# Performance work log

Hardware: AMD Instinct MI355X
Metric: run time of the kernel (lower is better)

## Reference

```python
import jax, jax.numpy as jnp
import numpy as np

B, L, D, M = 8, 4096, 512, 64


def setup_inputs() -> dict:
    key = jax.random.key(0)
    k1, k2, k3 = jax.random.split(key, 3)
    scale = 1.0 / (D * D)
    return {
        "q": jax.random.normal(k1, (B, L, D), dtype=jnp.float32),
        "w_real": scale * jax.random.normal(k2, (D, D, M), dtype=jnp.float32),
        "w_imag": scale * jax.random.normal(k3, (D, D, M), dtype=jnp.float32),
    }


def reference(q, w_real, w_imag):
    # q: [B, L, D]; weights: [D, D, modes]
    b, l, d = q.shape
    n_freq = l // 2 + 1
    q_ft = jnp.fft.rfft(q, axis=1)                      # [B, n_freq, D] complex64
    m = min(w_real.shape[-1], n_freq)
    W = w_real[..., :m] + 1j * w_imag[..., :m]          # [D, E, m] complex
    # Batched over modes: replaces the per-mode python loop with one einsum.
    out_m = jnp.einsum('bmd,dem->bme', q_ft[:, :m, :], W)  # [B, m, D]
    out_ft = jnp.zeros((b, n_freq, d), dtype=q_ft.dtype).at[:, :m, :].set(out_m)
    return jnp.fft.irfft(out_ft, n=l, axis=1)           # [B, L, D] float32
```

## Files before the change

kernel.cpp:

```cpp
#include <hip/hip_runtime.h>

#define B_ 8
#define L_ 4096
#define D_ 512
#define M_ 64

typedef __attribute__((ext_vector_type(8))) short bh8;
typedef __attribute__((ext_vector_type(4))) float f4;
typedef __attribute__((ext_vector_type(4))) unsigned u32x4;

__device__ inline unsigned short f2bf(float f) {
  unsigned u = __float_as_uint(f);
  return (unsigned short)((u + 0x7fffu + ((u >> 16) & 1u)) >> 16);
}
__device__ inline unsigned packbf(float lo, float hi) {
  return (unsigned)f2bf(lo) | ((unsigned)f2bf(hi) << 16);
}

__global__ void k_ftab(unsigned short* __restrict__ F) {
  int t = blockIdx.x * 256 + threadIdx.x;
  int r = t >> 12, l = t & 4095;
  int k = r & 63, part = r >> 6;
  int ph = (k * l) & (L_ - 1);
  double ang = 6.283185307179586476925286766559 * (double)ph / (double)L_;
  float v = part ? (float)(-sin(ang)) : (float)(cos(ang));
  F[t] = f2bf(v);
}

__global__ void k_gtab(unsigned short* __restrict__ G) {
  int t = blockIdx.x * 256 + threadIdx.x;
  int l = t >> 7, j = t & 127;
  int k = j & 63, part = j >> 6;
  int ph = (k * l) & (L_ - 1);
  double ang = 6.283185307179586476925286766559 * (double)ph / (double)L_;
  double ck = (k == 0 ? 1.0 : 2.0) / (double)L_;
  float v = part ? (float)(-ck * sin(ang)) : (float)(ck * cos(ang));
  G[t] = f2bf(v);
}

__global__ __launch_bounds__(512, 4) void k_dft_mfma(
    const float* __restrict__ q, const unsigned short* __restrict__ F,
    float* __restrict__ pQ) {
  int tid = threadIdx.x;
  int dt = blockIdx.x, b = blockIdx.y, kc = blockIdx.z;
  int d0 = dt * 64;
  int lbase = kc * 512;

  int w = tid >> 6, lane = tid & 63;
  int mh = w & 3, nc = w >> 2;
  int lr = lane & 15, kg = lane >> 4;

  f4 acc[2][2];
#pragma unroll
  for (int i = 0; i < 2; ++i)
#pragma unroll
    for (int j = 0; j < 2; ++j) { f4 z = {0.f, 0.f, 0.f, 0.f}; acc[i][j] = z; }

  const unsigned short* A0 = F + (size_t)(mh * 32 + lr) * 4096 + lbase + kg * 8;
  const unsigned short* A1 = A0 + (size_t)16 * 4096;
  const float* q0 = q + ((size_t)b * L_ + lbase + kg * 8) * D_ + d0 + nc * 32 + lr;

#pragma unroll 2
  for (int s = 0; s < 16; ++s) {
    const float* qs = q0 + (size_t)s * 32 * D_;
    float v0[8], v1[8];
#pragma unroll
    for (int j = 0; j < 8; ++j) {
      v0[j] = qs[(size_t)j * D_];
      v1[j] = qs[(size_t)j * D_ + 16];
    }
    union { u32x4 u; bh8 h; } bf0, bf1;
    bf0.u.x = packbf(v0[0], v0[1]); bf0.u.y = packbf(v0[2], v0[3]);
    bf0.u.z = packbf(v0[4], v0[5]); bf0.u.w = packbf(v0[6], v0[7]);
    bf1.u.x = packbf(v1[0], v1[1]); bf1.u.y = packbf(v1[2], v1[3]);
    bf1.u.z = packbf(v1[4], v1[5]); bf1.u.w = packbf(v1[6], v1[7]);
    bh8 af0 = *(const bh8*)(A0 + s * 32);
    bh8 af1 = *(const bh8*)(A1 + s * 32);
    acc[0][0] = __builtin_amdgcn_mfma_f32_16x16x32_bf16(af0, bf0.h, acc[0][0], 0, 0, 0);
    acc[0][1] = __builtin_amdgcn_mfma_f32_16x16x32_bf16(af0, bf1.h, acc[0][1], 0, 0, 0);
    acc[1][0] = __builtin_amdgcn_mfma_f32_16x16x32_bf16(af1, bf0.h, acc[1][0], 0, 0, 0);
    acc[1][1] = __builtin_amdgcn_mfma_f32_16x16x32_bf16(af1, bf1.h, acc[1][1], 0, 0, 0);
  }

#pragma unroll
  for (int mi = 0; mi < 2; ++mi) {
    int r = mh * 32 + mi * 16 + kg * 4;
#pragma unroll
    for (int ni = 0; ni < 2; ++ni) {
      int d = d0 + nc * 32 + ni * 16 + lr;
#pragma unroll
      for (int j = 0; j < 4; ++j)
        pQ[(((size_t)kc * 128 + (r + j)) * 8 + b) * 512 + d] = acc[mi][ni][j];
    }
  }
}

__global__ __launch_bounds__(256) void k_red2(const float* __restrict__ pQ,
                                              unsigned* __restrict__ Qbf) {
  int g = blockIdx.x * 256 + threadIdx.x;
  int dq = g & 127;
  int b = (g >> 7) & 7;
  int k = g >> 10;
  f4 sr = {0.f, 0.f, 0.f, 0.f}, si = {0.f, 0.f, 0.f, 0.f};
#pragma unroll
  for (int kc = 0; kc < 8; ++kc) {
    size_t base = (((size_t)kc * 128 + k) * 8 + b) * 512 + dq * 4;
    sr += *(const f4*)(pQ + base);
    si += *(const f4*)(pQ + base + (size_t)64 * 8 * 512);
  }
  u32x4 o;
  o.x = packbf(sr[0], si[0]); o.y = packbf(sr[1], si[1]);
  o.z = packbf(sr[2], si[2]); o.w = packbf(sr[3], si[3]);
  *(u32x4*)(Qbf + ((size_t)k * 8 + b) * 512 + dq * 4) = o;
}

__global__ __launch_bounds__(256, 5) void k_mix_mfma(
    const float* __restrict__ wr_, const float* __restrict__ wi_,
    const unsigned* __restrict__ Qbf, float* __restrict__ pOut) {
  __shared__ unsigned Wt[4096];

  int tid = threadIdx.x;
  int et = blockIdx.x, dc = blockIdx.y, kq = blockIdx.z;
  int e0 = et * 16, D0 = dc * 32, k0 = kq * 16;
  int w = tid >> 6, lane = tid & 63;
  int er = lane & 15, kg = lane >> 4;
  int part = er >> 3, b = er & 7;

  int se = tid & 15;
  int sk4 = (tid >> 4) & 3;
  int sdg = tid >> 6;

  f4 acc[4];
#pragma unroll
  for (int t = 0; t < 4; ++t) { f4 z = {0.f, 0.f, 0.f, 0.f}; acc[t] = z; }

#pragma unroll 1
  for (int r = 0; r < 2; ++r) {
    if (r) __syncthreads();
#pragma unroll
    for (int i = 0; i < 4; ++i) {
      int dl = sdg * 4 + i;
      size_t dd = (size_t)(D0 + r * 16 + dl);
      size_t gb = (dd * 512 + e0 + se) * 64 + k0 + sk4 * 4;
      float4 vr = *(const float4*)(wr_ + gb);
      float4 vi = *(const float4*)(wi_ + gb);
      int dp = dl ^ (sk4 << 2);
      unsigned* o = &Wt[(sk4 * 4) * 256 + se * 16 + dp];
      o[0]   = packbf(vr.x, vi.x);
      o[256] = packbf(vr.y, vi.y);
      o[512] = packbf(vr.z, vi.z);
      o[768] = packbf(vr.w, vi.w);
    }
    __syncthreads();
#pragma unroll
    for (int t = 0; t < 4; ++t) {
      int kl = w * 4 + t;
      int sw = (kl >> 2) << 2;
      union { u32x4 u; bh8 h; } av, bv;
      av.u = *(const u32x4*)&Wt[kl * 256 + er * 16 + ((kg * 4) ^ sw)];
      u32x4 qv = *(const u32x4*)(Qbf +
          ((size_t)(k0 + kl) * 8 + b) * 512 + D0 + r * 16 + kg * 4);
      if (part == 0) {
        bv.u.x = qv.x ^ 0x80000000u; bv.u.y = qv.y ^ 0x80000000u;
        bv.u.z = qv.z ^ 0x80000000u; bv.u.w = qv.w ^ 0x80000000u;
      } else {
        bv.u.x = (qv.x >> 16) | (qv.x << 16); bv.u.y = (qv.y >> 16) | (qv.y << 16);
        bv.u.z = (qv.z >> 16) | (qv.z << 16); bv.u.w = (qv.w >> 16) | (qv.w << 16);
      }
      acc[t] = __builtin_amdgcn_mfma_f32_16x16x32_bf16(av.h, bv.h, acc[t], 0, 0, 0);
    }
  }

#pragma unroll
  for (int t = 0; t < 4; ++t) {
    int kglob = k0 + w * 4 + t;
    size_t off = (size_t)dc * 524288 +
                 (((size_t)kglob * 2 + part) * 8 + b) * 512 + e0 + kg * 4;
    *(f4*)(pOut + off) = acc[t];
  }
}

__global__ __launch_bounds__(256) void k_psum2(const float* __restrict__ pOut,
                                               unsigned* __restrict__ Pw) {
  __shared__ float sP[128 * 33];
  int tid = threadIdx.x;
  int e0 = blockIdx.x * 32, b = blockIdx.y;
  {
    int e = tid & 31, kg4 = tid >> 5;
#pragma unroll
    for (int ii = 0; ii < 16; ++ii) {
      int col = kg4 * 16 + ii;
      int rkp = ((col & 63) << 1) | (col >> 6);
      float s = 0.f;
#pragma unroll
      for (int c = 0; c < 16; ++c)
        s += pOut[(size_t)c * 524288 + (size_t)rkp * 4096 + b * 512 + e0 + e];
      sP[col * 33 + e] = s;
    }
  }
  __syncthreads();
  {
    int e = tid >> 3, c = tid & 7;
    size_t wbase = (((size_t)b * 512 + e0 + e) * 128 + c * 16) >> 1;
#pragma unroll
    for (int ii = 0; ii < 8; ++ii) {
      int col = c * 16 + ii * 2;
      Pw[wbase + ii] = packbf(sP[col * 33 + e], sP[(col + 1) * 33 + e]);
    }
  }
}

#define LST 72
__global__ __launch_bounds__(256, 2) void k_inv_mfma(
    const short* __restrict__ G, const short* __restrict__ P,
    float* __restrict__ y) {
  __shared__ short lds[2 * 128 * LST];
  short* As = lds;
  short* Bs = lds + 128 * LST;

  int tid = threadIdx.x;
  int lt = blockIdx.x, et = blockIdx.y, b = blockIdx.z;
  int l0 = lt * 128, e0 = et * 128;

  int wv = tid >> 6, lane = tid & 63;
  int wrow = wv >> 1, wcol = wv & 1;
  int lr = lane & 15, kg = lane >> 4;

  const short* Gb = G + (size_t)l0 * 128;
  const short* Pb = P + (size_t)b * D_ * 128 + (size_t)e0 * 128;

  f4 acc[4][4];
#pragma unroll
  for (int mi = 0; mi < 4; ++mi)
#pragma unroll
    for (int ni = 0; ni < 4; ++ni) {
      f4 z = {0.f, 0.f, 0.f, 0.f};
      acc[mi][ni] = z;
    }

#pragma unroll
  for (int kh = 0; kh < 2; ++kh) {
    if (kh) __syncthreads();
#pragma unroll
    for (int i = 0; i < 4; ++i) {
      int idx = i * 256 + tid;
      int row = idx >> 3, c = idx & 7;
      *(uint4*)(As + row * LST + c * 8) =
          *(const uint4*)(Gb + (size_t)row * 128 + kh * 64 + c * 8);
      *(uint4*)(Bs + row * LST + c * 8) =
          *(const uint4*)(Pb + (size_t)row * 128 + kh * 64 + c * 8);
    }
    __syncthreads();

#pragma unroll
    for (int ks = 0; ks < 2; ++ks) {
      bh8 a[4], bf[4];
#pragma unroll
      for (int i = 0; i < 4; ++i) {
        a[i]  = *(const bh8*)(As + (wrow * 64 + i * 16 + lr) * LST + ks * 32 + kg * 8);
        bf[i] = *(const bh8*)(Bs + (wcol * 64 + i * 16 + lr) * LST + ks * 32 + kg * 8);
      }
#pragma unroll
      for (int mi = 0; mi < 4; ++mi)
#pragma unroll
        for (int ni = 0; ni < 4; ++ni)
          acc[mi][ni] = __builtin_amdgcn_mfma_f32_16x16x32_bf16(
              a[mi], bf[ni], acc[mi][ni], 0, 0, 0);
    }
  }

#pragma unroll
  for (int mi = 0; mi < 4; ++mi) {
    int lg = l0 + wrow * 64 + mi * 16 + kg * 4;
#pragma unroll
    for (int ni = 0; ni < 4; ++ni) {
      int e = e0 + wcol * 64 + ni * 16 + lr;
#pragma unroll
      for (int j = 0; j < 4; ++j)
        y[((size_t)b * L_ + (lg + j)) * D_ + e] = acc[mi][ni][j];
    }
  }
}

extern "C" void kernel_launch(void* const* d_in, const int* in_sizes, int n_in,
                              void* d_out, int out_size, void* d_ws, size_t ws_size,
                              hipStream_t stream) {
  const float* q  = (const float*)d_in[0];
  const float* wr = (const float*)d_in[1];
  const float* wi = (const float*)d_in[2];
  float* out = (float*)d_out;
  char* ws = (char*)d_ws;

  unsigned short* Fbf = (unsigned short*)ws;
  unsigned short* Gbf = (unsigned short*)(ws + (1u << 20));
  unsigned* Qbf       = (unsigned*)(ws + (2u << 20));
  unsigned* Pw        = (unsigned*)(ws + (3u << 20));

  float* pQ   = out;
  float* pOut = out;

  hipLaunchKernelGGL(k_ftab, dim3((128 * L_) / 256), dim3(256), 0, stream, Fbf);
  hipLaunchKernelGGL(k_gtab, dim3((L_ * 128) / 256), dim3(256), 0, stream, Gbf);
  hipLaunchKernelGGL(k_dft_mfma, dim3(8, 8, 8), dim3(512), 0, stream,
                     q, Fbf, pQ);
  hipLaunchKernelGGL(k_red2, dim3(65536 / 256), dim3(256), 0, stream, pQ, Qbf);
  hipLaunchKernelGGL(k_mix_mfma, dim3(32, 16, 4), dim3(256), 0, stream,
                     wr, wi, Qbf, pOut);
  hipLaunchKernelGGL(k_psum2, dim3(16, 8), dim3(256), 0, stream, pOut, Pw);
  hipLaunchKernelGGL(k_inv_mfma, dim3(L_ / 128, D_ / 128, B_), dim3(256), 0,
                     stream, (const short*)Gbf, (const short*)Pw, out);
}
```

Before: 113.7 us.

## Give each wave a private LDS weight tile in the mode-mixing kernel

Restructures the mode-mixing MFMA kernel so that each wave stages its own 16-mode by 16-channel weight slab into a private LDS buffer. Cross-wave __syncthreads is replaced by a waitcnt-based fence. Each wave now accumulates 16 MFMA tiles instead of 4, and the grid shrinks from 2048 to 512 blocks. The goal is to remove block-wide barriers and raise the number of global weight loads in flight per thread. In exchange it uses four times the LDS and more accumulator registers, which lowers occupancy, and it keeps 16 partial-sum slices over D.

```diff
diff --git a/kernel.cpp b/kernel.cpp
--- a/kernel.cpp
+++ b/kernel.cpp
@@ -114,52 +114,70 @@
   *(u32x4*)(Qbf + ((size_t)k * 8 + b) * 512 + dq * 4) = o;
 }
 
-__global__ __launch_bounds__(256, 5) void k_mix_mfma(
+__global__ __launch_bounds__(256, 2) void k_mix_mfma(
     const float* __restrict__ wr_, const float* __restrict__ wi_,
     const unsigned* __restrict__ Qbf, float* __restrict__ pOut) {
-  __shared__ unsigned Wt[4096];
+  __shared__ unsigned Wlds[4 * 4096];
 
   int tid = threadIdx.x;
-  int et = blockIdx.x, dc = blockIdx.y, kq = blockIdx.z;
-  int e0 = et * 16, D0 = dc * 32, k0 = kq * 16;
+  int et = blockIdx.x, dc = blockIdx.y, kh = blockIdx.z;
+  int e0 = et * 16;
   int w = tid >> 6, lane = tid & 63;
   int er = lane & 15, kg = lane >> 4;
   int part = er >> 3, b = er & 7;
-
-  int se = tid & 15;
-  int sk4 = (tid >> 4) & 3;
-  int sdg = tid >> 6;
-
-  f4 acc[4];
-#pragma unroll
-  for (int t = 0; t < 4; ++t) { f4 z = {0.f, 0.f, 0.f, 0.f}; acc[t] = z; }
+  int dh = w & 1;
+  int ksl = kh * 32 + (w >> 1) * 16;
+  unsigned* wbuf = Wlds + w * 4096;
+
+  int dL = lane >> 4;
+  int eL = (lane >> 2) & 3;
+  int kq = lane & 3;
+
+  f4 acc[16];
+#pragma unroll
+  for (int t = 0; t < 16; ++t) { f4 z = {0.f, 0.f, 0.f, 0.f}; acc[t] = z; }
+
+  const unsigned* qbase = Qbf + ((size_t)ksl * 8 + b) * 512 + kg * 4;
+
+#define DSFENCE() do {                                        \
+    asm volatile("s_waitcnt lgkmcnt(0)" ::: "memory");        \
+    __builtin_amdgcn_sched_barrier(0);                        \
+  } while (0)
 
 #pragma unroll 1
   for (int r = 0; r < 2; ++r) {
-    if (r) __syncthreads();
-#pragma unroll
-    for (int i = 0; i < 4; ++i) {
-      int dl = sdg * 4 + i;
-      size_t dd = (size_t)(D0 + r * 16 + dl);
-      size_t gb = (dd * 512 + e0 + se) * 64 + k0 + sk4 * 4;
-      float4 vr = *(const float4*)(wr_ + gb);
-      float4 vi = *(const float4*)(wi_ + gb);
-      int dp = dl ^ (sk4 << 2);
-      unsigned* o = &Wt[(sk4 * 4) * 256 + se * 16 + dp];
-      o[0]   = packbf(vr.x, vi.x);
-      o[256] = packbf(vr.y, vi.y);
-      o[512] = packbf(vr.z, vi.z);
-      o[768] = packbf(vr.w, vi.w);
-    }
-    __syncthreads();
-#pragma unroll
-    for (int t = 0; t < 4; ++t) {
-      int kl = w * 4 + t;
-      int sw = (kl >> 2) << 2;
+    int dbase = dc * 64 + r * 32 + dh * 16;
+
+#pragma unroll 1
+    for (int s = 0; s < 2; ++s) {
+      float4 vr[8], vi[8];
+#pragma unroll
+      for (int i = 0; i < 8; ++i) {
+        int d = dbase + s * 8 + dL + (i & 1) * 4;
+        int e = e0 + eL + (i >> 1) * 4;
+        size_t gb = ((size_t)d * 512 + e) * 64 + ksl + kq * 4;
+        vr[i] = *(const float4*)(wr_ + gb);
+        vi[i] = *(const float4*)(wi_ + gb);
+      }
+#pragma unroll
+      for (int i = 0; i < 8; ++i) {
+        int ee = eL + (i >> 1) * 4;
+        int dd = s * 8 + dL + (i & 1) * 4;
+        int ddp = dd ^ (kq << 2);
+        unsigned* o = wbuf + ee * 16 + ddp;
+        o[(kq * 4 + 0) * 256] = packbf(vr[i].x, vi[i].x);
+        o[(kq * 4 + 1) * 256] = packbf(vr[i].y, vi[i].y);
+        o[(kq * 4 + 2) * 256] = packbf(vr[i].z, vi[i].z);
+        o[(kq * 4 + 3) * 256] = packbf(vr[i].w, vi[i].w);
+      }
+    }
+    DSFENCE();
+
+#pragma unroll
+    for (int kl = 0; kl < 16; ++kl) {
       union { u32x4 u; bh8 h; } av, bv;
-      av.u = *(const u32x4*)&Wt[kl * 256 + er * 16 + ((kg * 4) ^ sw)];
-      u32x4 qv = *(const u32x4*)(Qbf +
-          ((size_t)(k0 + kl) * 8 + b) * 512 + D0 + r * 16 + kg * 4);
+      av.u = *(const u32x4*)(wbuf + kl * 256 + er * 16 + ((kg ^ (kl >> 2)) << 2));
+      u32x4 qv = *(const u32x4*)(qbase + (size_t)kl * 4096 + dbase);
       if (part == 0) {
         bv.u.x = qv.x ^ 0x80000000u; bv.u.y = qv.y ^ 0x80000000u;
         bv.u.z = qv.z ^ 0x80000000u; bv.u.w = qv.w ^ 0x80000000u;
@@ -167,16 +185,18 @@
         bv.u.x = (qv.x >> 16) | (qv.x << 16); bv.u.y = (qv.y >> 16) | (qv.y << 16);
         bv.u.z = (qv.z >> 16) | (qv.z << 16); bv.u.w = (qv.w >> 16) | (qv.w << 16);
       }
-      acc[t] = __builtin_amdgcn_mfma_f32_16x16x32_bf16(av.h, bv.h, acc[t], 0, 0, 0);
-    }
-  }
-
-#pragma unroll
-  for (int t = 0; t < 4; ++t) {
-    int kglob = k0 + w * 4 + t;
-    size_t off = (size_t)dc * 524288 +
+      acc[kl] = __builtin_amdgcn_mfma_f32_16x16x32_bf16(av.h, bv.h, acc[kl], 0, 0, 0);
+    }
+    DSFENCE();
+  }
+#undef DSFENCE
+
+#pragma unroll
+  for (int kl = 0; kl < 16; ++kl) {
+    int kglob = ksl + kl;
+    size_t off = (size_t)(dc * 2 + dh) * 524288 +
                  (((size_t)kglob * 2 + part) * 8 + b) * 512 + e0 + kg * 4;
-    *(f4*)(pOut + off) = acc[t];
+    *(f4*)(pOut + off) = acc[kl];
   }
 }
 
@@ -304,7 +324,7 @@
   hipLaunchKernelGGL(k_dft_mfma, dim3(8, 8, 8), dim3(512), 0, stream,
                      q, Fbf, pQ);
   hipLaunchKernelGGL(k_red2, dim3(65536 / 256), dim3(256), 0, stream, pQ, Qbf);
-  hipLaunchKernelGGL(k_mix_mfma, dim3(32, 16, 4), dim3(256), 0, stream,
+  hipLaunchKernelGGL(k_mix_mfma, dim3(32, 8, 2), dim3(256), 0, stream,
                      wr, wi, Qbf, pOut);
   hipLaunchKernelGGL(k_psum2, dim3(16, 8), dim3(256), 0, stream, pOut, Pw);
   hipLaunchKernelGGL(k_inv_mfma, dim3(L_ / 128, D_ / 128, B_), dim3(256), 0,
```

After: 111.8 us. About the same (-1.7%).
